# Optimization experiments

Measured on AMD Instinct MI355X. Metric: run time of the kernel, lower is better.

## Reference

```python
import jax, jax.numpy as jnp
import numpy as np

N = 4096          # number of polynomials in the ideal
E = 131072        # number of selectable (i, j) pairs
NUM_VARS = 16
NUM_MONOMIALS = 64
IN_DIM = NUM_VARS * NUM_MONOMIALS  # 1024, matches linear1.in_features exactly (no padding branch)
D = 256           # polys_embedding_dim


def _linear_params(key, out_f, in_f):
    kw, kb = jax.random.split(key)
    bound = 1.0 / np.sqrt(in_f)
    W = jax.random.uniform(kw, (out_f, in_f), jnp.float32, -bound, bound)
    b = jax.random.uniform(kb, (out_f,), jnp.float32, -bound, bound)
    return W, b


def setup_inputs() -> dict:
    key = jax.random.key(0)
    k_ideal, k1, k2, k3, k4 = jax.random.split(key, 5)
    ideal = jax.random.normal(k_ideal, (N, NUM_MONOMIALS, NUM_VARS), jnp.float32)
    # unique (i, j) pairs so scatter-set semantics match the torch loop exactly
    flat = np.random.default_rng(0).choice(N * N, size=E, replace=False)
    edge_index = jnp.asarray(np.stack([flat // N, flat % N], axis=1).astype(np.int64))
    W1, b1 = _linear_params(k1, D, IN_DIM)        # linear1
    W2, b2 = _linear_params(k2, D, D)             # linear2
    We1, be1 = _linear_params(k3, D, 2 * D)       # evaluation1
    We2, be2 = _linear_params(k4, 1, D)           # evaluation2
    return {"ideal": ideal, "edge_index": edge_index,
            "W1": W1, "b1": b1, "W2": W2, "b2": b2,
            "We1": We1, "be1": be1, "We2": We2, "be2": be2}


def reference(ideal, edge_index, W1, b1, W2, b2, We1, be1, We2, be2):
    n = ideal.shape[0]
    # per-node polynomial embedding (identical math to per-edge recomputation in torch)
    x = ideal.reshape(n, -1)                              # [N, IN_DIM]
    h = jnp.maximum(x @ W1.T + b1, 0.0) @ W2.T + b2       # [N, D]
    # edge-wise gather -> tiny MLP -> scalar score
    hi = h[edge_index[:, 0]]                              # [E, D]
    hj = h[edge_index[:, 1]]                              # [E, D]
    e = jnp.concatenate([hi, hj], axis=-1)                # [E, 2D]
    s = jnp.maximum(e @ We1.T + be1, 0.0) @ We2.T + be2   # [E, 1]
    # scatter scores into sparse [N, N] matrix, -inf elsewhere, then global softmax
    vals = jnp.full((n, n), -jnp.inf, dtype=s.dtype)
    vals = vals.at[edge_index[:, 0], edge_index[:, 1]].set(s[:, 0])
    probs = jax.nn.softmax(vals.reshape(-1))              # [N*N]
    return probs
```

## Files before the change

### kernel.cpp

```cpp
#include <hip/hip_runtime.h>
#include <hip/hip_bf16.h>


typedef unsigned short u16;
typedef unsigned int   u32;
typedef __attribute__((ext_vector_type(8))) short bf16x8;
typedef __attribute__((ext_vector_type(4))) float f32x4;

#define N_NODES 4096
#define E_EDGES 131072
#define AS1 __attribute__((address_space(1)))
#define AS3 __attribute__((address_space(3)))

__device__ __forceinline__ u16 f2bf(float f) {
    u32 u = __float_as_uint(f);
    return (u16)((u + 0x7FFFu + ((u >> 16) & 1u)) >> 16);
}
__device__ __forceinline__ float bflo(u32 w) { return __uint_as_float(w << 16); }
__device__ __forceinline__ float bfhi(u32 w) { return __uint_as_float(w & 0xffff0000u); }

__device__ __forceinline__ void fill_shard(float4* __restrict__ out4,
                                           int shard, int fb, int tid)
{
    float4* op = out4 + (size_t)shard * 1048576 + (size_t)fb * 8192 + tid;
    const float4 z = {0.f, 0.f, 0.f, 0.f};
    #pragma unroll 8
    for (int q = 0; q < 32; ++q)
        op[(size_t)q * 256] = z;
}

__device__ __forceinline__ void pack_body(const float* __restrict__ in,
                                          u16* __restrict__ hi, int K, int kcs, int gid)
{
    const int r   = gid & 63;
    const int kb  = (gid >> 6) & 7;
    const int pkc = gid >> 9;
    const int kc  = pkc & ((1 << kcs) - 1);
    const int p   = pkc >> kcs;
    const size_t row = ((size_t)p << 6) | r;
    const int k0 = (kc << 6) | (kb << 3);

    const float* src = in + row * (size_t)K + k0;
    const float4 v0 = *(const float4*)src;
    const float4 v1 = *(const float4*)(src + 4);
    const float vv[8] = {v0.x, v0.y, v0.z, v0.w, v1.x, v1.y, v1.z, v1.w};

    u32 hw[4];
    #pragma unroll
    for (int q = 0; q < 4; ++q)
        hw[q] = (u32)f2bf(vv[2 * q]) | ((u32)f2bf(vv[2 * q + 1]) << 16);
    uint4 hv = {hw[0], hw[1], hw[2], hw[3]};
    *(uint4*)(hi + (size_t)gid * 8) = hv;
}

__global__ __launch_bounds__(256)
void prep_all(const float* __restrict__ W1, const float* __restrict__ We1,
              const float* __restrict__ W2, const float* __restrict__ b2,
              const float* __restrict__ be1,
              u16* __restrict__ w1h, u16* __restrict__ wabh,
              float* __restrict__ bab, float4* __restrict__ out4)
{
    const int bid = blockIdx.x;
    if (bid < 128) {
        pack_body(W1, w1h, 1024, 4, bid * 256 + threadIdx.x);
    } else if (bid < 192) {
        const int r0 = (bid - 128) * 8;
        const int c  = threadIdx.x;
        float acc[8] = {};
        for (int k = 0; k < 256; ++k) {
            const float w2 = W2[k * 256 + c];
            #pragma unroll
            for (int j = 0; j < 8; ++j) {
                const int r = r0 + j;
                acc[j] += We1[(size_t)(r & 255) * 512 + ((r >> 8) << 8) + k] * w2;
            }
        }
        const int kc = c >> 6, kb = (c >> 3) & 7, e = c & 7;
        #pragma unroll
        for (int j = 0; j < 8; ++j) {
            const int r = r0 + j;
            wabh[(((((size_t)(r >> 6) << 2) + kc) << 3) + kb) * 512 + (size_t)(r & 63) * 8 + e]
                = f2bf(acc[j]);
        }
    } else if (bid < 194) {
        const int r = (bid - 192) * 256 + threadIdx.x;
        const int i = r & 255;
        const int koff = (r >> 8) << 8;
        float acc = (r < 256) ? be1[i] : 0.0f;
        for (int k = 0; k < 256; k += 4) {
            const float4 w = *(const float4*)(We1 + (size_t)i * 512 + koff + k);
            const float4 b = *(const float4*)(b2 + k);
            acc += w.x * b.x + w.y * b.y + w.z * b.z + w.w * b.w;
        }
        bab[r] = acc;
    } else {
        fill_shard(out4, 0, bid - 194, threadIdx.x);
    }
}

__global__ __launch_bounds__(512)
void gemm12(const float* __restrict__ X, const u16* __restrict__ w1h,
            const u16* __restrict__ wabh, const float* __restrict__ b1,
            const float* __restrict__ bab, u16* __restrict__ ABout,
            float4* __restrict__ out4)
{
    const int b = blockIdx.x;
    if (b >= 256) {
        const int fb = b - 256;
        float4* op = out4 + 1048576 + (size_t)fb * 8192 + threadIdx.x;
        const float4 z = {0.f, 0.f, 0.f, 0.f};
        #pragma unroll 8
        for (int q = 0; q < 16; ++q)
            op[(size_t)q * 512] = z;
        return;
    }

    __shared__ u16 Xp[17408];
    __shared__ u16 H1[4096];
    const int tid  = threadIdx.x;
    const int wv   = tid >> 6;
    const int lane = tid & 63;
    const int kq   = lane >> 4;
    const int r16  = lane & 15;
    const int R0   = b << 4;

    #pragma unroll
    for (int q = 0; q < 4; ++q) {
        const int gid = (q << 9) + tid;
        const int kb  = gid & 127;
        const int row = gid >> 7;
        const float* src = X + (size_t)(R0 + row) * 1024 + (kb << 3);
        const float4 v0 = *(const float4*)src;
        const float4 v1 = *(const float4*)(src + 4);
        const float vv[8] = {v0.x, v0.y, v0.z, v0.w, v1.x, v1.y, v1.z, v1.w};
        u32 hw[4];
        #pragma unroll
        for (int e = 0; e < 4; ++e)
            hw[e] = (u32)f2bf(vv[2 * e]) | ((u32)f2bf(vv[2 * e + 1]) << 16);
        uint4 hv = {hw[0], hw[1], hw[2], hw[3]};
        *(uint4*)&Xp[kb * 136 + (row << 3)] = hv;
    }
    __syncthreads();

    const int pn1 = wv >> 1;
    const u16* pw1 = w1h + (((size_t)pn1 * 16) << 12);

    f32x4 acc1[2];
    acc1[0] = (f32x4){0.f, 0.f, 0.f, 0.f};
    acc1[1] = (f32x4){0.f, 0.f, 0.f, 0.f};

    #pragma unroll 4
    for (int t = 0; t < 16; ++t) {
        #pragma unroll
        for (int s = 0; s < 2; ++s) {
            const int kb  = (s << 2) + kq;
            const int kbg = (t << 3) + kb;
            const bf16x8 af = *(const bf16x8*)&Xp[kbg * 136 + (r16 << 3)];
            #pragma unroll
            for (int n = 0; n < 2; ++n) {
                const int c0 = ((wv & 1) << 5) + (n << 4);
                const bf16x8 bf = *(const bf16x8*)
                    (pw1 + ((size_t)t << 12) + (kb << 9) + ((size_t)(c0 + r16) << 3));
                acc1[n] = __builtin_amdgcn_mfma_f32_16x16x32_bf16(af, bf, acc1[n], 0, 0, 0);
            }
        }
    }

    #pragma unroll
    for (int n = 0; n < 2; ++n) {
        const int col = (wv << 5) + (n << 4) + r16;
        const float bv = b1[col];
        const int kb2 = col >> 3;
        #pragma unroll
        for (int j = 0; j < 4; ++j) {
            const float v = fmaxf(acc1[n][j] + bv, 0.0f);
            H1[(((kb2 << 4) + (kq << 2) + j) << 3) + (col & 7)] = f2bf(v);
        }
    }
    __syncthreads();

    const u16* pw2 = wabh + (((size_t)wv * 4) << 12);
    f32x4 acc2[4];
    #pragma unroll
    for (int n = 0; n < 4; ++n) acc2[n] = (f32x4){0.f, 0.f, 0.f, 0.f};

    #pragma unroll
    for (int t = 0; t < 4; ++t) {
        #pragma unroll
        for (int s = 0; s < 2; ++s) {
            const int kb = (s << 2) + kq;
            const int kb32 = (t << 3) + kb;
            const bf16x8 af = *(const bf16x8*)&H1[((kb32 << 4) + r16) << 3];
            #pragma unroll
            for (int n = 0; n < 4; ++n) {
                const bf16x8 bf = *(const bf16x8*)
                    (pw2 + ((size_t)t << 12) + (kb << 9) + ((size_t)((n << 4) + r16) << 3));
                acc2[n] = __builtin_amdgcn_mfma_f32_16x16x32_bf16(af, bf, acc2[n], 0, 0, 0);
            }
        }
    }

    #pragma unroll
    for (int n = 0; n < 4; ++n) {
        const int col = (wv << 6) + (n << 4) + r16;
        const float bv = bab[col];
        #pragma unroll
        for (int j = 0; j < 4; ++j) {
            const int row = R0 + (kq << 2) + j;
            ABout[(size_t)row * 512 + col] = f2bf(acc2[n][j] + bv);
        }
    }
}

__global__ __launch_bounds__(256)
void edge_z(const u16* __restrict__ AB, const int* __restrict__ idx,
            const float* __restrict__ We2, const float* __restrict__ be2p,
            float* __restrict__ vbuf, float* __restrict__ part,
            float4* __restrict__ out4)
{
    const int bid = blockIdx.x;
    const int tid = threadIdx.x;

    if (bid >= 2048) {
        fill_shard(out4, 3, bid - 2048, tid);
        return;
    }

    __shared__ float sm[256];
    const int cb   = bid;
    const int lane = tid & 63;
    const int sub  = lane >> 5;
    const int l5   = lane & 31;
    const int wid  = (cb * 256 + tid) >> 6;
    const float be2 = be2p[0];

    float w2v[8];
    #pragma unroll
    for (int q = 0; q < 2; ++q) {
        const float4 w = ((const float4*)We2)[l5 * 2 + q];
        w2v[q * 4 + 0] = w.x; w2v[q * 4 + 1] = w.y;
        w2v[q * 4 + 2] = w.z; w2v[q * 4 + 3] = w.w;
    }

    float zloc = 0.0f;
    #pragma unroll
    for (int it = 0; it < 8; ++it) {
        const int e = (wid << 1) + sub + (it << 14);
        const int src = idx[2 * e];
        const int dst = idx[2 * e + 1];
        const uint4 av = *(const uint4*)(AB + ((size_t)src << 9) + (l5 << 3));
        const uint4 bv = *(const uint4*)(AB + ((size_t)dst << 9) + 256 + (l5 << 3));
        const u32 aw[4] = {av.x, av.y, av.z, av.w};
        const u32 bw[4] = {bv.x, bv.y, bv.z, bv.w};
        float p = 0.0f;
        #pragma unroll
        for (int q = 0; q < 4; ++q) {
            p += fmaxf(bflo(aw[q]) + bflo(bw[q]), 0.0f) * w2v[2 * q];
            p += fmaxf(bfhi(aw[q]) + bfhi(bw[q]), 0.0f) * w2v[2 * q + 1];
        }
        #pragma unroll
        for (int m = 16; m > 0; m >>= 1)
            p += __shfl_xor(p, m, 64);
        const float v = expf(p + be2);
        if (l5 == 0) {
            vbuf[e] = v;
            zloc += v;
        }
    }
    sm[tid] = zloc;
    __syncthreads();
    for (int st = 128; st > 0; st >>= 1) {
        if (tid < st) sm[tid] += sm[tid + st];
        __syncthreads();
    }
    if (tid == 0) part[cb] = sm[0];
}

__global__ __launch_bounds__(256)
void scatter_probs(const float* __restrict__ vbuf, const int* __restrict__ idx,
                   const float* __restrict__ part, float* __restrict__ out, int n)
{
    __shared__ float sm[256];
    float a = part[threadIdx.x];
    #pragma unroll
    for (int k = 1; k < 8; ++k)
        a += part[threadIdx.x + k * 256];
    sm[threadIdx.x] = a;
    __syncthreads();
    for (int st = 128; st > 0; st >>= 1) {
        if (threadIdx.x < st) sm[threadIdx.x] += sm[threadIdx.x + st];
        __syncthreads();
    }
    const float Z = sm[0];
    const int e = blockIdx.x * 256 + threadIdx.x;
    if (e < n)
        out[(size_t)idx[2 * e] * N_NODES + idx[2 * e + 1]] = vbuf[e] / Z;
}

extern "C" void kernel_launch(void* const* d_in, const int* in_sizes, int n_in,
                              void* d_out, int out_size, void* d_ws, size_t ws_size,
                              hipStream_t stream)
{
    const float* ideal = (const float*)d_in[0];
    const int*   idx   = (const int*)d_in[1];
    const float* W1    = (const float*)d_in[2];
    const float* b1    = (const float*)d_in[3];
    const float* W2    = (const float*)d_in[4];
    const float* b2    = (const float*)d_in[5];
    const float* We1   = (const float*)d_in[6];
    const float* be1   = (const float*)d_in[7];
    const float* We2   = (const float*)d_in[8];
    const float* be2   = (const float*)d_in[9];
    float* out = (float*)d_out;

    char* Wb = (char*)d_ws;
    u16*   w1h  = (u16*)(Wb);
    u16*   wabh = (u16*)(Wb + (512u << 10));
    float* bab  = (float*)(Wb + (768u << 10));
    u16*   ABbf = (u16*)(Wb + (1u << 20));
    float* vbuf = (float*)(Wb + (6u << 20));
    float* part = vbuf + E_EDGES;

    prep_all<<<322, 256, 0, stream>>>(W1, We1, W2, b2, be1,
                                      w1h, wabh, bab, (float4*)out);

    gemm12<<<512, 512, 0, stream>>>(ideal, w1h, wabh, b1, bab, ABbf, (float4*)out);

    edge_z<<<2176, 256, 0, stream>>>(ABbf, idx, We2, be2, vbuf, part, (float4*)out);
    scatter_probs<<<512, 256, 0, stream>>>(vbuf, idx, part, out, E_EDGES);
}
```

Measured before the change: 65.95 us.

## Fuse edge scoring and scatter via grid-wide spin barrier, drop vbuf round-trip

```diff
diff --git a/kernel.cpp b/kernel.cpp
--- a/kernel.cpp
+++ b/kernel.cpp
@@ -58,7 +58,8 @@
               const float* __restrict__ W2, const float* __restrict__ b2,
               const float* __restrict__ be1,
               u16* __restrict__ w1h, u16* __restrict__ wabh,
-              float* __restrict__ bab, float4* __restrict__ out4)
+              float* __restrict__ bab, u32* __restrict__ cnt,
+              float4* __restrict__ out4)
 {
     const int bid = blockIdx.x;
     if (bid < 128) {
@@ -94,6 +95,8 @@
         }
         bab[r] = acc;
     } else {
+        if (bid == 194 && threadIdx.x == 0)
+            __hip_atomic_store(cnt, 0u, __ATOMIC_RELAXED, __HIP_MEMORY_SCOPE_AGENT);
         fill_shard(out4, 0, bid - 194, threadIdx.x);
     }
 }
@@ -212,26 +215,19 @@
     }
 }
 
-__global__ __launch_bounds__(256)
-void edge_z(const u16* __restrict__ AB, const int* __restrict__ idx,
-            const float* __restrict__ We2, const float* __restrict__ be2p,
-            float* __restrict__ vbuf, float* __restrict__ part,
-            float4* __restrict__ out4)
-{
-    const int bid = blockIdx.x;
-    const int tid = threadIdx.x;
-
-    if (bid >= 2048) {
-        fill_shard(out4, 3, bid - 2048, tid);
-        return;
-    }
-
+__global__ __launch_bounds__(256, 4)
+void edge_scatter(const u16* __restrict__ AB, const int* __restrict__ idx,
+                  const float* __restrict__ We2, const float* __restrict__ be2p,
+                  float* __restrict__ part, u32* __restrict__ cnt,
+                  float* __restrict__ out)
+{
     __shared__ float sm[256];
-    const int cb   = bid;
+    const int bid  = blockIdx.x;
+    const int tid  = threadIdx.x;
     const int lane = tid & 63;
-    const int sub  = lane >> 5;
+    const int hw   = tid >> 5;
     const int l5   = lane & 31;
-    const int wid  = (cb * 256 + tid) >> 6;
+    const int ebase = (bid << 7) + (hw << 4);
     const float be2 = be2p[0];
 
     float w2v[8];
@@ -242,10 +238,10 @@
         w2v[q * 4 + 2] = w.z; w2v[q * 4 + 3] = w.w;
     }
 
-    float zloc = 0.0f;
-    #pragma unroll
-    for (int it = 0; it < 8; ++it) {
-        const int e = (wid << 1) + sub + (it << 14);
+    float vmine = 0.0f;
+    #pragma unroll
+    for (int i = 0; i < 16; ++i) {
+        const int e = ebase + i;
         const int src = idx[2 * e];
         const int dst = idx[2 * e + 1];
         const uint4 av = *(const uint4*)(AB + ((size_t)src << 9) + (l5 << 3));
@@ -262,39 +258,45 @@
         for (int m = 16; m > 0; m >>= 1)
             p += __shfl_xor(p, m, 64);
         const float v = expf(p + be2);
-        if (l5 == 0) {
-            vbuf[e] = v;
-            zloc += v;
-        }
-    }
-    sm[tid] = zloc;
+        if (l5 == i) vmine = v;
+    }
+
+    sm[tid] = vmine;
     __syncthreads();
     for (int st = 128; st > 0; st >>= 1) {
         if (tid < st) sm[tid] += sm[tid + st];
         __syncthreads();
     }
-    if (tid == 0) part[cb] = sm[0];
-}
-
-__global__ __launch_bounds__(256)
-void scatter_probs(const float* __restrict__ vbuf, const int* __restrict__ idx,
-                   const float* __restrict__ part, float* __restrict__ out, int n)
-{
-    __shared__ float sm[256];
-    float a = part[threadIdx.x];
-    #pragma unroll
-    for (int k = 1; k < 8; ++k)
-        a += part[threadIdx.x + k * 256];
-    sm[threadIdx.x] = a;
+    if (tid == 0) {
+        __hip_atomic_store(&part[bid], sm[0], __ATOMIC_RELAXED, __HIP_MEMORY_SCOPE_AGENT);
+        asm volatile("s_waitcnt vmcnt(0)" ::: "memory");
+        __hip_atomic_fetch_add(cnt, 1u, __ATOMIC_RELAXED, __HIP_MEMORY_SCOPE_AGENT);
+        int spins = 0;
+        while (__hip_atomic_load(cnt, __ATOMIC_RELAXED, __HIP_MEMORY_SCOPE_AGENT) < 1024u
+               && spins < (1 << 26)) {
+            __builtin_amdgcn_s_sleep(2);
+            ++spins;
+        }
+        (void)__hip_atomic_load(cnt, __ATOMIC_ACQUIRE, __HIP_MEMORY_SCOPE_AGENT);
+    }
+    __syncthreads();
+
+    float a = __hip_atomic_load(&part[tid], __ATOMIC_RELAXED, __HIP_MEMORY_SCOPE_AGENT)
+            + __hip_atomic_load(&part[tid + 256], __ATOMIC_RELAXED, __HIP_MEMORY_SCOPE_AGENT)
+            + __hip_atomic_load(&part[tid + 512], __ATOMIC_RELAXED, __HIP_MEMORY_SCOPE_AGENT)
+            + __hip_atomic_load(&part[tid + 768], __ATOMIC_RELAXED, __HIP_MEMORY_SCOPE_AGENT);
+    sm[tid] = a;
     __syncthreads();
     for (int st = 128; st > 0; st >>= 1) {
-        if (threadIdx.x < st) sm[threadIdx.x] += sm[threadIdx.x + st];
+        if (tid < st) sm[tid] += sm[tid + st];
         __syncthreads();
     }
     const float Z = sm[0];
-    const int e = blockIdx.x * 256 + threadIdx.x;
-    if (e < n)
-        out[(size_t)idx[2 * e] * N_NODES + idx[2 * e + 1]] = vbuf[e] / Z;
+
+    if (l5 < 16) {
+        const int e = ebase + l5;
+        out[(size_t)idx[2 * e] * N_NODES + idx[2 * e + 1]] = vmine / Z;
+    }
 }
 
 extern "C" void kernel_launch(void* const* d_in, const int* in_sizes, int n_in,
@@ -318,14 +320,13 @@
     u16*   wabh = (u16*)(Wb + (512u << 10));
     float* bab  = (float*)(Wb + (768u << 10));
     u16*   ABbf = (u16*)(Wb + (1u << 20));
-    float* vbuf = (float*)(Wb + (6u << 20));
-    float* part = vbuf + E_EDGES;
+    float* part = (float*)(Wb + (6u << 20));
+    u32*   cnt  = (u32*)(Wb + (6u << 20) + 8192);
 
     prep_all<<<322, 256, 0, stream>>>(W1, We1, W2, b2, be1,
-                                      w1h, wabh, bab, (float4*)out);
-
-    gemm12<<<512, 512, 0, stream>>>(ideal, w1h, wabh, b1, bab, ABbf, (float4*)out);
-
-    edge_z<<<2176, 256, 0, stream>>>(ABbf, idx, We2, be2, vbuf, part, (float4*)out);
-    scatter_probs<<<512, 256, 0, stream>>>(vbuf, idx, part, out, E_EDGES);
-}
+                                      w1h, wabh, bab, cnt, (float4*)out);
+
+    gemm12<<<640, 512, 0, stream>>>(ideal, w1h, wabh, b1, bab, ABbf, (float4*)out);
+
+    edge_scatter<<<1024, 256, 0, stream>>>(ABbf, idx, We2, be2, part, cnt, out);
+}
```

New measurement: 121.2 us. 1.84x slower.
